# Kernel tuning notes

Measured on AMD Instinct MI355X. Metric: run time of the kernel, lower is better.

The kernel has to match this reference:

```python
import jax, jax.numpy as jnp
import numpy as np

D_MODEL = 1024
NUM_HEADS = 16
HEAD_DIM = D_MODEL // NUM_HEADS


def setup_inputs() -> dict:
    key = jax.random.key(0)
    ks = jax.random.split(key, 12)
    B, Lq, Lkv = 4, 1024, 2048
    s = 1.0 / np.sqrt(D_MODEL)
    inp = {
        "decoder_hidden": jax.random.normal(ks[0], (B, Lq, D_MODEL), jnp.float32),
        "encoder_hidden": jax.random.normal(ks[1], (B, Lkv, D_MODEL), jnp.float32),
        "encoder_mask": jnp.ones((B, 1, 1, Lkv), jnp.int32),
        "Wq": jax.random.normal(ks[2], (D_MODEL, D_MODEL), jnp.float32) * s,
        "bq": jnp.zeros((D_MODEL,), jnp.float32),
        "Wk": jax.random.normal(ks[3], (D_MODEL, D_MODEL), jnp.float32) * s,
        "bk": jnp.zeros((D_MODEL,), jnp.float32),
        "Wv": jax.random.normal(ks[4], (D_MODEL, D_MODEL), jnp.float32) * s,
        "bv": jnp.zeros((D_MODEL,), jnp.float32),
        "Wo": jax.random.normal(ks[5], (D_MODEL, D_MODEL), jnp.float32) * s,
        "bo": jnp.zeros((D_MODEL,), jnp.float32),
    }
    return inp


def _split_heads(x):
    # [B, L, D] -> [B, H, L, Dh]
    B, L, _ = x.shape
    return x.reshape(B, L, NUM_HEADS, HEAD_DIM).transpose(0, 2, 1, 3)


def reference(decoder_hidden, encoder_hidden, encoder_mask,
              Wq, bq, Wk, bk, Wv, bv, Wo, bo):
    B, Lq, _ = decoder_hidden.shape
    q = _split_heads(decoder_hidden @ Wq.T + bq)   # [B,H,Lq,Dh]
    k = _split_heads(encoder_hidden @ Wk.T + bk)   # [B,H,Lkv,Dh]
    v = _split_heads(encoder_hidden @ Wv.T + bv)   # [B,H,Lkv,Dh]
    scale = 1.0 / np.sqrt(HEAD_DIM).astype(np.float32)
    scores = jnp.einsum('bhqd,bhkd->bhqk', q, k) * scale  # [B,H,Lq,Lkv]
    scores = jnp.where(encoder_mask == 0, jnp.float32(-jnp.inf), scores)
    attn = jax.nn.softmax(scores, axis=-1)  # dropout is identity in eval mode
    out = jnp.einsum('bhqk,bhkd->bhqd', attn, v)  # [B,H,Lq,Dh]
    out = out.transpose(0, 2, 1, 3).reshape(B, Lq, D_MODEL)
    return out @ Wo.T + bo
```

## Files before the change

### kernel.cpp

```cpp
#include <hip/hip_runtime.h>
#include <hip/hip_bf16.h>
#include <stdint.h>
#include <math.h>

#define B_   4
#define H_   16
#define LQ_  1024
#define LKV_ 2048
#define DM_  1024
#define DH_  64

typedef __attribute__((ext_vector_type(8))) __bf16 bf16x8;
typedef __attribute__((ext_vector_type(4))) float  f32x4;
typedef __attribute__((ext_vector_type(16))) float f32x16;
typedef __attribute__((ext_vector_type(8))) short  short8;
typedef __attribute__((ext_vector_type(2))) unsigned uint2v;

__device__ __forceinline__ void gload_lds16(const void* g, void* l) {
  __builtin_amdgcn_global_load_lds(
      (const __attribute__((address_space(1))) void*)g,
      (__attribute__((address_space(3))) void*)l, 16, 0, 0);
}

__device__ __forceinline__ void drain_vmem() {
  asm volatile("s_waitcnt vmcnt(0)" ::: "memory");
  __builtin_amdgcn_sched_barrier(0);
}

#if __has_builtin(__builtin_amdgcn_exp2f)
__device__ __forceinline__ float EXP2(float x) { return __builtin_amdgcn_exp2f(x); }
#else
__device__ __forceinline__ float EXP2(float x) {
  float r; asm("v_exp_f32 %0, %1" : "=v"(r) : "v"(x)); return r;
}
#endif

#if __has_builtin(__builtin_amdgcn_permlane32_swap)
__device__ __forceinline__ void xswap(unsigned& a, unsigned& b) {
  uint2v r = __builtin_amdgcn_permlane32_swap(a, b, false, false);
  a = r[0]; b = r[1];
}
#else
__device__ __forceinline__ void xswap(unsigned& a, unsigned& b) {
  unsigned xa = (unsigned)__shfl_xor((int)a, 32);
  unsigned xb = (unsigned)__shfl_xor((int)b, 32);
  bool hi = (threadIdx.x & 32) != 0;
  unsigned na = hi ? xb : a;
  unsigned nb = hi ? b : xa;
  a = na; b = nb;
}
#endif

__device__ __forceinline__ unsigned pack2(float a, float b) {
  unsigned lo = (unsigned)__bfloat16_as_ushort(__float2bfloat16(a));
  unsigned hi = (unsigned)__bfloat16_as_ushort(__float2bfloat16(b));
  return lo | (hi << 16);
}

struct CastArgs {
  const float* src[6];
  __hip_bfloat16* dst[6];
  int n[6];
};

__global__ void cast_multi(CastArgs a) {
  int seg = blockIdx.y;
  int n = a.n[seg];
  int i = (blockIdx.x * blockDim.x + threadIdx.x) * 8;
  if (i >= n) return;
  const float* s = a.src[seg] + i;
  float4 x = *(const float4*)s;
  float4 y = *(const float4*)(s + 4);
  union { short8 v; __hip_bfloat16 h[8]; } u;
  u.h[0] = __float2bfloat16(x.x); u.h[1] = __float2bfloat16(x.y);
  u.h[2] = __float2bfloat16(x.z); u.h[3] = __float2bfloat16(x.w);
  u.h[4] = __float2bfloat16(y.x); u.h[5] = __float2bfloat16(y.y);
  u.h[6] = __float2bfloat16(y.z); u.h[7] = __float2bfloat16(y.w);
  *(short8*)(a.dst[seg] + i) = u.v;
}

__global__ void mask_mul(const int* __restrict__ msk, __hip_bfloat16* __restrict__ mb, int n) {
  int i = blockIdx.x * blockDim.x + threadIdx.x;
  if (i < n) mb[i] = __float2bfloat16(msk[i] ? 1.0f : 0.0f);
}

template<int MODE>
__global__ __launch_bounds__(256, 3)
void gemm_bt(const __hip_bfloat16* __restrict__ A,
             const __hip_bfloat16* __restrict__ Bt,
             const float* __restrict__ bias,
             void* __restrict__ Cout, int M, int N, int K) {
  __shared__ __hip_bfloat16 lA[2][128 * 64];
  __shared__ __hip_bfloat16 lB[2][64 * 64];
  const int tid = threadIdx.x;
  const int lane = tid & 63, wv = tid >> 6;
  const int l16 = lane & 15, lg = lane >> 4;
  const int wm = wv >> 1, wn = wv & 1;
  const int tileM = blockIdx.y * 128, tileN = blockIdx.x * 64;
  const int KB = K * 2;

  f32x4 acc[4][2] = {};
  const int o0 = wv * 1024 + lane * 16;

  auto GSTAGE = [&](int bi, int kt) {
#pragma unroll
    for (int j = 0; j < 4; ++j) {
      int o = o0 + j * 4096;
      int row = o >> 7, col = (o & 127) ^ ((row & 7) << 4);
      gload_lds16((const char*)A + (size_t)(tileM + row) * KB + kt * 2 + col,
                  (char*)lA[bi] + wv * 1024 + j * 4096);
    }
#pragma unroll
    for (int j = 0; j < 2; ++j) {
      int o = o0 + j * 4096;
      int row = o >> 7, col = (o & 127) ^ ((row & 7) << 4);
      gload_lds16((const char*)Bt + (size_t)(tileN + row) * KB + kt * 2 + col,
                  (char*)lB[bi] + wv * 1024 + j * 4096);
    }
  };

  GSTAGE(0, 0);
  drain_vmem();
  __syncthreads();
  int buf = 0;
  const int NT = K / 64;
  for (int t = 0; t < NT; ++t) {
    if (t + 1 < NT) GSTAGE(buf ^ 1, (t + 1) * 64);
    bf16x8 af[4][2], bfr[2][2];
#pragma unroll
    for (int mt = 0; mt < 4; ++mt) {
      const int row = wm * 64 + mt * 16 + l16;
      const int sw = (row & 7) << 4;
#pragma unroll
      for (int kk = 0; kk < 2; ++kk)
        af[mt][kk] = *(const bf16x8*)((const char*)lA[buf] + row * 128 + ((kk * 64 + lg * 16) ^ sw));
    }
#pragma unroll
    for (int nt = 0; nt < 2; ++nt) {
      const int row = wn * 32 + nt * 16 + l16;
      const int sw = (row & 7) << 4;
#pragma unroll
      for (int kk = 0; kk < 2; ++kk)
        bfr[nt][kk] = *(const bf16x8*)((const char*)lB[buf] + row * 128 + ((kk * 64 + lg * 16) ^ sw));
    }
#pragma unroll
    for (int kk = 0; kk < 2; ++kk)
#pragma unroll
      for (int mt = 0; mt < 4; ++mt)
#pragma unroll
        for (int nt = 0; nt < 2; ++nt)
          acc[mt][nt] = __builtin_amdgcn_mfma_f32_16x16x32_bf16(af[mt][kk], bfr[nt][kk], acc[mt][nt], 0, 0, 0);
    drain_vmem();
    __syncthreads();
    buf ^= 1;
  }

#pragma unroll
  for (int mt = 0; mt < 4; ++mt) {
#pragma unroll
    for (int nt = 0; nt < 2; ++nt) {
      int col = tileN + wn * 32 + nt * 16 + l16;
      float bcol = bias[col];
      int row0 = tileM + wm * 64 + mt * 16 + lg * 4;
      f32x4 a = acc[mt][nt];
#pragma unroll
      for (int r = 0; r < 4; ++r) {
        int row = row0 + r;
        float v = a[r] + bcol;
        if (MODE == 0) {
          ((__hip_bfloat16*)Cout)[(size_t)row * N + col] = __float2bfloat16(v);
        } else {
          ((float*)Cout)[(size_t)row * N + col] = v;
        }
      }
    }
  }
}

__global__ __launch_bounds__(256, 3)
void gemm_kv(const __hip_bfloat16* __restrict__ A,
             const __hip_bfloat16* __restrict__ Bt,
             const float* __restrict__ bk,
             const float* __restrict__ bv,
             __hip_bfloat16* __restrict__ Kout,
             __hip_bfloat16* __restrict__ Vtout,
             const int* __restrict__ vmask) {
  const int K = 1024;
  __shared__ __hip_bfloat16 lA[2][128 * 32];
  __shared__ __hip_bfloat16 lB[2][128 * 32];
  const int tid = threadIdx.x;
  const int lane = tid & 63, wv = tid >> 6;
  const int l16 = lane & 15, lg = lane >> 4;
  const int wm = wv >> 1, wn = wv & 1;
  const int tileM = blockIdx.y * 128, tileN = blockIdx.x * 128;
  const int KB = K * 2;

  f32x4 acc[4][4] = {};
  const int o0 = tid * 16;

  auto GSTAGE = [&](int bi, int kt) {
#pragma unroll
    for (int j = 0; j < 2; ++j) {
      int o = o0 + j * 4096;
      int row = o >> 6, col = (o & 63) ^ ((row & 3) << 4);
      gload_lds16((const char*)A + (size_t)(tileM + row) * KB + kt * 2 + col,
                  (char*)lA[bi] + (tid & 192) * 16 + j * 4096);
    }
#pragma unroll
    for (int j = 0; j < 2; ++j) {
      int o = o0 + j * 4096;
      int row = o >> 6, col = (o & 63) ^ ((row & 3) << 4);
      gload_lds16((const char*)Bt + (size_t)(tileN + row) * KB + kt * 2 + col,
                  (char*)lB[bi] + (tid & 192) * 16 + j * 4096);
    }
  };

  GSTAGE(0, 0);
  drain_vmem();
  __syncthreads();
  int buf = 0;
  const int NT = K / 32;
  for (int t = 0; t < NT; ++t) {
    if (t + 1 < NT) GSTAGE(buf ^ 1, (t + 1) * 32);
    bf16x8 af[4], bfr[4];
#pragma unroll
    for (int mt = 0; mt < 4; ++mt) {
      const int row = wm * 64 + mt * 16 + l16;
      af[mt] = *(const bf16x8*)((const char*)lA[buf] + row * 64 + ((lg * 16) ^ ((row & 3) << 4)));
    }
#pragma unroll
    for (int nt = 0; nt < 4; ++nt) {
      const int row = wn * 64 + nt * 16 + l16;
      bfr[nt] = *(const bf16x8*)((const char*)lB[buf] + row * 64 + ((lg * 16) ^ ((row & 3) << 4)));
    }
#pragma unroll
    for (int mt = 0; mt < 4; ++mt)
#pragma unroll
      for (int nt = 0; nt < 4; ++nt)
        acc[mt][nt] = __builtin_amdgcn_mfma_f32_16x16x32_bf16(af[mt], bfr[nt], acc[mt][nt], 0, 0, 0);
    drain_vmem();
    __syncthreads();
    buf ^= 1;
  }

#pragma unroll
  for (int mt = 0; mt < 4; ++mt) {
#pragma unroll
    for (int nt = 0; nt < 4; ++nt) {
      int col = tileN + wn * 64 + nt * 16 + l16;
      int row0 = tileM + wm * 64 + mt * 16 + lg * 4;
      f32x4 a = acc[mt][nt];
      if (col < 1024) {
        float bc = bk[col];
#pragma unroll
        for (int r = 0; r < 4; ++r) {
          int row = row0 + r;
          Kout[(size_t)row * 1024 + col] = __float2bfloat16(a[r] + bc);
        }
      } else {
        int cv = col - 1024;
        float bc = bv[cv];
#pragma unroll
        for (int r = 0; r < 4; ++r) {
          int row = row0 + r;
          int b = row >> 11, kv = row & 2047;
          float v = a[r] + bc;
          if (!vmask[b * 2048 + kv]) v = 0.0f;
          Vtout[((size_t)(b * 1024 + cv)) * 2048 + kv] = __float2bfloat16(v);
        }
      }
    }
  }
}

__global__ __launch_bounds__(256, 2)
void attn_fwd(const __hip_bfloat16* __restrict__ Qg,
              const __hip_bfloat16* __restrict__ Kg,
              const __hip_bfloat16* __restrict__ Vt,
              const __hip_bfloat16* __restrict__ mkb,
              __hip_bfloat16* __restrict__ AO) {
  __shared__ __hip_bfloat16 lK[2][64 * 64];
  __shared__ __hip_bfloat16 lV[2][64 * 64];
  const int tid = threadIdx.x, lane = tid & 63, wv = tid >> 6;
  const int l32 = lane & 31, h = lane >> 5;

  const int blk = blockIdx.x;
  const int c8 = blk & 7, j = blk >> 3;
  const int g8 = c8 * 8 + (j & 7);
  const int qi = j >> 3;
  const int hd = g8 & 15, b = g8 >> 4;
  const int qb = qi * 128;
  const int q0 = qb + wv * 32;

  const char* qbase = (const char*)Qg +
      ((size_t)(b * LQ_ + q0 + l32) * DM_ + hd * DH_ + h * 8) * 2;
  bf16x8 qf[4];
#pragma unroll
  for (int dk = 0; dk < 4; ++dk) qf[dk] = *(const bf16x8*)(qbase + dk * 32);

  f32x16 o[2] = {};
  f32x16 l_acc = {};
  float m2 = -1e30f;
  const float S2 = 0.18033688f;
  const __hip_bfloat16* mrow = mkb + b * LKV_;
  const char* Kbase = (const char*)Kg + ((size_t)(b * LKV_) * DM_ + hd * DH_) * 2;
  const char* Vbase = (const char*)Vt + ((size_t)((b * H_ + hd) * DH_)) * LKV_ * 2;

  const int ofs = wv * 1024 + lane * 16;
  const int r0 = ofs >> 7, c0s = (ofs & 127) ^ ((r0 & 7) << 4);
  const int ofs1 = ofs + 4096;
  const int r1 = ofs1 >> 7, c1s = (ofs1 & 127) ^ ((r1 & 7) << 4);

  auto STAGE = [&](int bi, int kv0) {
    gload_lds16(Kbase + (size_t)(kv0 + r0) * 2048 + c0s, (char*)lK[bi] + wv * 1024);
    gload_lds16(Kbase + (size_t)(kv0 + r1) * 2048 + c1s, (char*)lK[bi] + 4096 + wv * 1024);
    gload_lds16(Vbase + (size_t)r0 * 4096 + kv0 * 2 + c0s, (char*)lV[bi] + wv * 1024);
    gload_lds16(Vbase + (size_t)r1 * 4096 + kv0 * 2 + c1s, (char*)lV[bi] + 4096 + wv * 1024);
  };

  STAGE(0, 0);
  drain_vmem();
  __syncthreads();
  int buf = 0;

  for (int it = 0; it < LKV_ / 64; ++it) {
    const int kv0 = it * 64;
    if (it + 1 < LKV_ / 64) STAGE(buf ^ 1, kv0 + 64);

    f32x16 z[2];
#pragma unroll
    for (int t = 0; t < 2; ++t) {
      z[t] = {};
      const int row = t * 32 + l32;
      const int sw = (row & 7) << 4;
      const char* kp = (const char*)lK[buf] + row * 128;
      __builtin_amdgcn_s_setprio(1);
#pragma unroll
      for (int dk = 0; dk < 4; ++dk) {
        bf16x8 kf = *(const bf16x8*)(kp + ((dk * 32 + h * 16) ^ sw));
        z[t] = __builtin_amdgcn_mfma_f32_32x32x16_bf16(kf, qf[dk], z[t], 0, 0, 0);
      }
      __builtin_amdgcn_s_setprio(0);
    }

    f32x16 zm;
#pragma unroll
    for (int g = 0; g < 16; ++g) zm[g] = fmaxf(z[0][g], z[1][g]);
    float m0 = fmaxf(fmaxf(zm[0], zm[1]), fmaxf(zm[2], zm[3]));
    float m1 = fmaxf(fmaxf(zm[4], zm[5]), fmaxf(zm[6], zm[7]));
    float m4 = fmaxf(fmaxf(zm[8], zm[9]), fmaxf(zm[10], zm[11]));
    float m5 = fmaxf(fmaxf(zm[12], zm[13]), fmaxf(zm[14], zm[15]));
    float mx = fmaxf(fmaxf(m0, m1), fmaxf(m4, m5));
    mx = fmaxf(mx, __shfl_xor(mx, 32));
    float mx2 = mx * S2;

    if (!__all(mx2 - m2 <= 11.5416f)) {
      float mn = fmaxf(m2, mx2);
      float alpha = EXP2(m2 - mn);
      m2 = mn;
#pragma unroll
      for (int g = 0; g < 16; ++g) {
        float a2 = __shfl(alpha, (g & 3) + 8 * (g >> 2) + 4 * h);
        o[0][g] *= a2;
        o[1][g] *= a2;
        l_acc[g] *= a2;
      }
    }

    const float negm2 = -m2;
    unsigned pk[2][4][2];
#pragma unroll
    for (int t = 0; t < 2; ++t)
#pragma unroll
      for (int s = 0; s < 4; ++s) {
        float p0 = EXP2(fmaf(z[t][s * 4 + 0], S2, negm2));
        float p1 = EXP2(fmaf(z[t][s * 4 + 1], S2, negm2));
        float p2 = EXP2(fmaf(z[t][s * 4 + 2], S2, negm2));
        float p3 = EXP2(fmaf(z[t][s * 4 + 3], S2, negm2));
        pk[t][s][0] = pack2(p0, p1);
        pk[t][s][1] = pack2(p2, p3);
      }

#pragma unroll
    for (int c = 0; c < 4; ++c) {
      const int t = c >> 1, cc = c & 1;
      unsigned w0 = pk[t][2 * cc + 0][0], w1 = pk[t][2 * cc + 0][1];
      unsigned w2 = pk[t][2 * cc + 1][0], w3 = pk[t][2 * cc + 1][1];
      xswap(w0, w2);
      xswap(w1, w3);
      union { unsigned w[4]; bf16x8 v; } au;
      au.w[0] = w0; au.w[1] = w1; au.w[2] = w2; au.w[3] = w3;
      bf16x8 mb8 = *(const bf16x8*)(mrow + kv0 + c * 16 + h * 8);
      __builtin_amdgcn_s_setprio(1);
#pragma unroll
      for (int dt = 0; dt < 2; ++dt) {
        const int row = dt * 32 + l32;
        const int sw = (row & 7) << 4;
        bf16x8 vf = *(const bf16x8*)((const char*)lV[buf] + row * 128 + ((c * 32 + h * 16) ^ sw));
        o[dt] = __builtin_amdgcn_mfma_f32_32x32x16_bf16(au.v, vf, o[dt], 0, 0, 0);
      }
      l_acc = __builtin_amdgcn_mfma_f32_32x32x16_bf16(au.v, mb8, l_acc, 0, 0, 0);
      __builtin_amdgcn_s_setprio(0);
    }
    drain_vmem();
    __syncthreads();
    buf ^= 1;
  }

#pragma unroll
  for (int dt = 0; dt < 2; ++dt)
#pragma unroll
    for (int g = 0; g < 16; ++g) {
      int q = (g & 3) + 8 * (g >> 2) + 4 * h;
      AO[(size_t)(b * LQ_ + qb + wv * 32 + q) * DM_ + hd * DH_ + dt * 32 + l32] =
          __float2bfloat16(o[dt][g] / l_acc[g]);
    }
}

extern "C" void kernel_launch(void* const* d_in, const int* in_sizes, int n_in,
                              void* d_out, int out_size, void* d_ws, size_t ws_size,
                              hipStream_t stream) {
  const float* dec = (const float*)d_in[0];
  const float* enc = (const float*)d_in[1];
  const int*   msk = (const int*)d_in[2];
  const float* Wq = (const float*)d_in[3];
  const float* bq = (const float*)d_in[4];
  const float* Wk = (const float*)d_in[5];
  const float* bk = (const float*)d_in[6];
  const float* Wv = (const float*)d_in[7];
  const float* bv = (const float*)d_in[8];
  const float* Wo = (const float*)d_in[9];
  const float* bo = (const float*)d_in[10];

  char* ws = (char*)d_ws;
  __hip_bfloat16* decB = (__hip_bfloat16*)(ws);
  __hip_bfloat16* encB = (__hip_bfloat16*)(ws + 8388608);
  __hip_bfloat16* WqB  = (__hip_bfloat16*)(ws + 25165824);
  __hip_bfloat16* WkvB = (__hip_bfloat16*)(ws + 27262976);
  __hip_bfloat16* WoB  = (__hip_bfloat16*)(ws + 31457280);
  __hip_bfloat16* Qb   = (__hip_bfloat16*)(ws + 33554432);
  __hip_bfloat16* Kb   = (__hip_bfloat16*)(ws + 41943040);
  __hip_bfloat16* Vtb  = (__hip_bfloat16*)(ws + 58720256);
  __hip_bfloat16* AO   = (__hip_bfloat16*)(ws + 75497472);
  __hip_bfloat16* mk2  = (__hip_bfloat16*)(ws + 83886080);

  CastArgs ca;
  ca.src[0] = dec; ca.dst[0] = decB;             ca.n[0] = 4096 * 1024;
  ca.src[1] = enc; ca.dst[1] = encB;             ca.n[1] = 8192 * 1024;
  ca.src[2] = Wq;  ca.dst[2] = WqB;              ca.n[2] = 1024 * 1024;
  ca.src[3] = Wk;  ca.dst[3] = WkvB;             ca.n[3] = 1024 * 1024;
  ca.src[4] = Wv;  ca.dst[4] = WkvB + 1048576;   ca.n[4] = 1024 * 1024;
  ca.src[5] = Wo;  ca.dst[5] = WoB;              ca.n[5] = 1024 * 1024;
  cast_multi<<<dim3(4096, 6), dim3(256), 0, stream>>>(ca);
  mask_mul<<<dim3(32), dim3(256), 0, stream>>>(msk, mk2, B_ * LKV_);

  gemm_bt<0><<<dim3(16, 32), dim3(256), 0, stream>>>(decB, WqB, bq, (void*)Qb, 4096, 1024, 1024);
  gemm_kv<<<dim3(16, 64), dim3(256), 0, stream>>>(encB, WkvB, bk, bv, Kb, Vtb, msk);

  attn_fwd<<<dim3(512), dim3(256), 0, stream>>>(Qb, Kb, Vtb, mk2, AO);

  gemm_bt<2><<<dim3(16, 32), dim3(256), 0, stream>>>(AO, WoB, bo, d_out, 4096, 1024, 1024);
}
```

Measured before the change: 187.4 us.

## Replace LDS-staged attention with single-wave blocks loading K/V into registers

The attention kernel drops its shared-memory double buffer and block barriers. Each 64-thread block now handles 32 queries and reads K and V tiles straight from global memory into registers, prefetching the next K tile while the current one computes. This removes LDS traffic and synchronisation, but each wave now fetches K/V on its own, with no sharing across the four waves that used to share a tile. That raises global/L2 traffic and may expose more load latency.

```diff
diff --git a/kernel.cpp b/kernel.cpp
--- a/kernel.cpp
+++ b/kernel.cpp
@@ -273,15 +273,103 @@
   }
 }
 
-__global__ __launch_bounds__(256, 2)
-void attn_fwd(const __hip_bfloat16* __restrict__ Qg,
+__device__ __forceinline__ void attn_tile(
+    const char* Kb_, const char* Vb_, const __hip_bfloat16* mrow,
+    int kv0, int l32, int h,
+    const bf16x8 (&qf)[4], bf16x8 (&kf_cur)[2][4], bf16x8 (&kf_nxt)[2][4],
+    f32x16 (&o_)[2], f32x16& l_acc, float& m2) {
+  const float S2 = 0.18033688f;
+
+  bf16x8 vf[4][2], mf[4];
+#pragma unroll
+  for (int c = 0; c < 4; ++c) {
+#pragma unroll
+    for (int dt = 0; dt < 2; ++dt)
+      vf[c][dt] = *(const bf16x8*)(Vb_ + (size_t)(dt * 32 + l32) * 4096 + kv0 * 2 + c * 32 + h * 16);
+    mf[c] = *(const bf16x8*)(mrow + kv0 + c * 16 + h * 8);
+  }
+
+  f32x16 z[2];
+#pragma unroll
+  for (int t = 0; t < 2; ++t) {
+    z[t] = {};
+    __builtin_amdgcn_s_setprio(1);
+#pragma unroll
+    for (int dk = 0; dk < 4; ++dk)
+      z[t] = __builtin_amdgcn_mfma_f32_32x32x16_bf16(kf_cur[t][dk], qf[dk], z[t], 0, 0, 0);
+    __builtin_amdgcn_s_setprio(0);
+  }
+
+  const int kvn = (kv0 < (LKV_ - 64)) ? kv0 + 64 : 0;
+#pragma unroll
+  for (int t = 0; t < 2; ++t)
+#pragma unroll
+    for (int dk = 0; dk < 4; ++dk)
+      kf_nxt[t][dk] = *(const bf16x8*)(Kb_ + (size_t)(kvn + t * 32 + l32) * 2048 + dk * 32 + h * 16);
+
+  f32x16 zm;
+#pragma unroll
+  for (int g = 0; g < 16; ++g) zm[g] = fmaxf(z[0][g], z[1][g]);
+  float m0 = fmaxf(fmaxf(zm[0], zm[1]), fmaxf(zm[2], zm[3]));
+  float m1 = fmaxf(fmaxf(zm[4], zm[5]), fmaxf(zm[6], zm[7]));
+  float m4 = fmaxf(fmaxf(zm[8], zm[9]), fmaxf(zm[10], zm[11]));
+  float m5 = fmaxf(fmaxf(zm[12], zm[13]), fmaxf(zm[14], zm[15]));
+  float mx = fmaxf(fmaxf(m0, m1), fmaxf(m4, m5));
+  mx = fmaxf(mx, __shfl_xor(mx, 32));
+  float mx2 = mx * S2;
+
+  if (!__all(mx2 - m2 <= 11.5416f)) {
+    float mn = fmaxf(m2, mx2);
+    float alpha = EXP2(m2 - mn);
+    m2 = mn;
+#pragma unroll
+    for (int g = 0; g < 16; ++g) {
+      float a2 = __shfl(alpha, (g & 3) + 8 * (g >> 2) + 4 * h);
+      o_[0][g] *= a2;
+      o_[1][g] *= a2;
+      l_acc[g] *= a2;
+    }
+  }
+
+  const float negm2 = -m2;
+  unsigned pk[2][4][2];
+#pragma unroll
+  for (int t = 0; t < 2; ++t)
+#pragma unroll
+    for (int s = 0; s < 4; ++s) {
+      float p0 = EXP2(fmaf(z[t][s * 4 + 0], S2, negm2));
+      float p1 = EXP2(fmaf(z[t][s * 4 + 1], S2, negm2));
+      float p2 = EXP2(fmaf(z[t][s * 4 + 2], S2, negm2));
+      float p3 = EXP2(fmaf(z[t][s * 4 + 3], S2, negm2));
+      pk[t][s][0] = pack2(p0, p1);
+      pk[t][s][1] = pack2(p2, p3);
+    }
+
+#pragma unroll
+  for (int c = 0; c < 4; ++c) {
+    const int t = c >> 1, cc = c & 1;
+    unsigned w0 = pk[t][2 * cc + 0][0], w1 = pk[t][2 * cc + 0][1];
+    unsigned w2 = pk[t][2 * cc + 1][0], w3 = pk[t][2 * cc + 1][1];
+    xswap(w0, w2);
+    xswap(w1, w3);
+    union { unsigned w[4]; bf16x8 v; } au;
+    au.w[0] = w0; au.w[1] = w1; au.w[2] = w2; au.w[3] = w3;
+    __builtin_amdgcn_s_setprio(1);
+#pragma unroll
+    for (int dt = 0; dt < 2; ++dt)
+      o_[dt] = __builtin_amdgcn_mfma_f32_32x32x16_bf16(au.v, vf[c][dt], o_[dt], 0, 0, 0);
+    l_acc = __builtin_amdgcn_mfma_f32_32x32x16_bf16(au.v, mf[c], l_acc, 0, 0, 0);
+    __builtin_amdgcn_s_setprio(0);
+  }
+}
+
+__global__ __launch_bounds__(64, 2)
+void attn_reg(const __hip_bfloat16* __restrict__ Qg,
               const __hip_bfloat16* __restrict__ Kg,
               const __hip_bfloat16* __restrict__ Vt,
               const __hip_bfloat16* __restrict__ mkb,
               __hip_bfloat16* __restrict__ AO) {
-  __shared__ __hip_bfloat16 lK[2][64 * 64];
-  __shared__ __hip_bfloat16 lV[2][64 * 64];
-  const int tid = threadIdx.x, lane = tid & 63, wv = tid >> 6;
+  const int lane = threadIdx.x & 63;
   const int l32 = lane & 31, h = lane >> 5;
 
   const int blk = blockIdx.x;
@@ -289,8 +377,7 @@
   const int g8 = c8 * 8 + (j & 7);
   const int qi = j >> 3;
   const int hd = g8 & 15, b = g8 >> 4;
-  const int qb = qi * 128;
-  const int q0 = qb + wv * 32;
+  const int q0 = qi * 32;
 
   const char* qbase = (const char*)Qg +
       ((size_t)(b * LQ_ + q0 + l32) * DM_ + hd * DH_ + h * 8) * 2;
@@ -298,113 +385,24 @@
 #pragma unroll
   for (int dk = 0; dk < 4; ++dk) qf[dk] = *(const bf16x8*)(qbase + dk * 32);
 
-  f32x16 o[2] = {};
+  const char* Kb_ = (const char*)Kg + ((size_t)(b * LKV_) * DM_ + hd * DH_) * 2;
+  const char* Vb_ = (const char*)Vt + ((size_t)((b * H_ + hd) * DH_)) * LKV_ * 2;
+  const __hip_bfloat16* mrow = mkb + b * LKV_;
+
+  bf16x8 kfA[2][4], kfB[2][4];
+#pragma unroll
+  for (int t = 0; t < 2; ++t)
+#pragma unroll
+    for (int dk = 0; dk < 4; ++dk)
+      kfA[t][dk] = *(const bf16x8*)(Kb_ + (size_t)(t * 32 + l32) * 2048 + dk * 32 + h * 16);
+
+  f32x16 o_[2] = {};
   f32x16 l_acc = {};
   float m2 = -1e30f;
-  const float S2 = 0.18033688f;
-  const __hip_bfloat16* mrow = mkb + b * LKV_;
-  const char* Kbase = (const char*)Kg + ((size_t)(b * LKV_) * DM_ + hd * DH_) * 2;
-  const char* Vbase = (const char*)Vt + ((size_t)((b * H_ + hd) * DH_)) * LKV_ * 2;
-
-  const int ofs = wv * 1024 + lane * 16;
-  const int r0 = ofs >> 7, c0s = (ofs & 127) ^ ((r0 & 7) << 4);
-  const int ofs1 = ofs + 4096;
-  const int r1 = ofs1 >> 7, c1s = (ofs1 & 127) ^ ((r1 & 7) << 4);
-
-  auto STAGE = [&](int bi, int kv0) {
-    gload_lds16(Kbase + (size_t)(kv0 + r0) * 2048 + c0s, (char*)lK[bi] + wv * 1024);
-    gload_lds16(Kbase + (size_t)(kv0 + r1) * 2048 + c1s, (char*)lK[bi] + 4096 + wv * 1024);
-    gload_lds16(Vbase + (size_t)r0 * 4096 + kv0 * 2 + c0s, (char*)lV[bi] + wv * 1024);
-    gload_lds16(Vbase + (size_t)r1 * 4096 + kv0 * 2 + c1s, (char*)lV[bi] + 4096 + wv * 1024);
-  };
-
-  STAGE(0, 0);
-  drain_vmem();
-  __syncthreads();
-  int buf = 0;
-
-  for (int it = 0; it < LKV_ / 64; ++it) {
-    const int kv0 = it * 64;
-    if (it + 1 < LKV_ / 64) STAGE(buf ^ 1, kv0 + 64);
-
-    f32x16 z[2];
-#pragma unroll
-    for (int t = 0; t < 2; ++t) {
-      z[t] = {};
-      const int row = t * 32 + l32;
-      const int sw = (row & 7) << 4;
-      const char* kp = (const char*)lK[buf] + row * 128;
-      __builtin_amdgcn_s_setprio(1);
-#pragma unroll
-      for (int dk = 0; dk < 4; ++dk) {
-        bf16x8 kf = *(const bf16x8*)(kp + ((dk * 32 + h * 16) ^ sw));
-        z[t] = __builtin_amdgcn_mfma_f32_32x32x16_bf16(kf, qf[dk], z[t], 0, 0, 0);
-      }
-      __builtin_amdgcn_s_setprio(0);
-    }
-
-    f32x16 zm;
-#pragma unroll
-    for (int g = 0; g < 16; ++g) zm[g] = fmaxf(z[0][g], z[1][g]);
-    float m0 = fmaxf(fmaxf(zm[0], zm[1]), fmaxf(zm[2], zm[3]));
-    float m1 = fmaxf(fmaxf(zm[4], zm[5]), fmaxf(zm[6], zm[7]));
-    float m4 = fmaxf(fmaxf(zm[8], zm[9]), fmaxf(zm[10], zm[11]));
-    float m5 = fmaxf(fmaxf(zm[12], zm[13]), fmaxf(zm[14], zm[15]));
-    float mx = fmaxf(fmaxf(m0, m1), fmaxf(m4, m5));
-    mx = fmaxf(mx, __shfl_xor(mx, 32));
-    float mx2 = mx * S2;
-
-    if (!__all(mx2 - m2 <= 11.5416f)) {
-      float mn = fmaxf(m2, mx2);
-      float alpha = EXP2(m2 - mn);
-      m2 = mn;
-#pragma unroll
-      for (int g = 0; g < 16; ++g) {
-        float a2 = __shfl(alpha, (g & 3) + 8 * (g >> 2) + 4 * h);
-        o[0][g] *= a2;
-        o[1][g] *= a2;
-        l_acc[g] *= a2;
-      }
-    }
-
-    const float negm2 = -m2;
-    unsigned pk[2][4][2];
-#pragma unroll
-    for (int t = 0; t < 2; ++t)
-#pragma unroll
-      for (int s = 0; s < 4; ++s) {
-        float p0 = EXP2(fmaf(z[t][s * 4 + 0], S2, negm2));
-        float p1 = EXP2(fmaf(z[t][s * 4 + 1], S2, negm2));
-        float p2 = EXP2(fmaf(z[t][s * 4 + 2], S2, negm2));
-        float p3 = EXP2(fmaf(z[t][s * 4 + 3], S2, negm2));
-        pk[t][s][0] = pack2(p0, p1);
-        pk[t][s][1] = pack2(p2, p3);
-      }
-
-#pragma unroll
-    for (int c = 0; c < 4; ++c) {
-      const int t = c >> 1, cc = c & 1;
-      unsigned w0 = pk[t][2 * cc + 0][0], w1 = pk[t][2 * cc + 0][1];
-      unsigned w2 = pk[t][2 * cc + 1][0], w3 = pk[t][2 * cc + 1][1];
-      xswap(w0, w2);
-      xswap(w1, w3);
-      union { unsigned w[4]; bf16x8 v; } au;
-      au.w[0] = w0; au.w[1] = w1; au.w[2] = w2; au.w[3] = w3;
-      bf16x8 mb8 = *(const bf16x8*)(mrow + kv0 + c * 16 + h * 8);
-      __builtin_amdgcn_s_setprio(1);
-#pragma unroll
-      for (int dt = 0; dt < 2; ++dt) {
-        const int row = dt * 32 + l32;
-        const int sw = (row & 7) << 4;
-        bf16x8 vf = *(const bf16x8*)((const char*)lV[buf] + row * 128 + ((c * 32 + h * 16) ^ sw));
-        o[dt] = __builtin_amdgcn_mfma_f32_32x32x16_bf16(au.v, vf, o[dt], 0, 0, 0);
-      }
-      l_acc = __builtin_amdgcn_mfma_f32_32x32x16_bf16(au.v, mb8, l_acc, 0, 0, 0);
-      __builtin_amdgcn_s_setprio(0);
-    }
-    drain_vmem();
-    __syncthreads();
-    buf ^= 1;
+
+  for (int it = 0; it < LKV_ / 64; it += 2) {
+    attn_tile(Kb_, Vb_, mrow, it * 64,      l32, h, qf, kfA, kfB, o_, l_acc, m2);
+    attn_tile(Kb_, Vb_, mrow, it * 64 + 64, l32, h, qf, kfB, kfA, o_, l_acc, m2);
   }
 
 #pragma unroll
@@ -412,8 +410,8 @@
 #pragma unroll
     for (int g = 0; g < 16; ++g) {
       int q = (g & 3) + 8 * (g >> 2) + 4 * h;
-      AO[(size_t)(b * LQ_ + qb + wv * 32 + q) * DM_ + hd * DH_ + dt * 32 + l32] =
-          __float2bfloat16(o[dt][g] / l_acc[g]);
+      AO[(size_t)(b * LQ_ + q0 + q) * DM_ + hd * DH_ + dt * 32 + l32] =
+          __float2bfloat16(o_[dt][g] / l_acc[g]);
     }
 }
 
@@ -457,7 +455,7 @@
   gemm_bt<0><<<dim3(16, 32), dim3(256), 0, stream>>>(decB, WqB, bq, (void*)Qb, 4096, 1024, 1024);
   gemm_kv<<<dim3(16, 64), dim3(256), 0, stream>>>(encB, WkvB, bk, bv, Kb, Vtb, msk);
 
-  attn_fwd<<<dim3(512), dim3(256), 0, stream>>>(Qb, Kb, Vtb, mk2, AO);
+  attn_reg<<<dim3(2048), dim3(64), 0, stream>>>(Qb, Kb, Vtb, mk2, AO);
 
   gemm_bt<2><<<dim3(16, 32), dim3(256), 0, stream>>>(AO, WoB, bo, d_out, 4096, 1024, 1024);
 }
```

After: 247.3 us. 1.32x slower.

## Merge Q and KV projections into one launch; widen attention KV tile to 128

Applied to the files above, without the earlier changes.

The Q projection GEMM is folded into the KV GEMM kernel as one 1-D grid of 1280 blocks. The first 256 blocks compute Q tiles and the rest compute K/V tiles, which removes a launch and lets the two GEMMs fill the machine together. The attention kernel now stages 128 KV rows per iteration instead of 64. This halves the loop trips and the barriers, and does the softmax max/rescale once per 128 keys. In exchange it doubles LDS use (64KB across both buffers) and increases register pressure, which may lower occupancy.

```diff
diff --git a/kernel.cpp b/kernel.cpp
--- a/kernel.cpp
+++ b/kernel.cpp
@@ -178,13 +178,17 @@
 }
 
 __global__ __launch_bounds__(256, 3)
-void gemm_kv(const __hip_bfloat16* __restrict__ A,
-             const __hip_bfloat16* __restrict__ Bt,
-             const float* __restrict__ bk,
-             const float* __restrict__ bv,
-             __hip_bfloat16* __restrict__ Kout,
-             __hip_bfloat16* __restrict__ Vtout,
-             const int* __restrict__ vmask) {
+void gemm_qkv(const __hip_bfloat16* __restrict__ decB,
+              const __hip_bfloat16* __restrict__ WqB,
+              const float* __restrict__ bq,
+              const __hip_bfloat16* __restrict__ encB,
+              const __hip_bfloat16* __restrict__ WkvB,
+              const float* __restrict__ bk,
+              const float* __restrict__ bv,
+              __hip_bfloat16* __restrict__ Qout,
+              __hip_bfloat16* __restrict__ Kout,
+              __hip_bfloat16* __restrict__ Vtout,
+              const int* __restrict__ vmask) {
   const int K = 1024;
   __shared__ __hip_bfloat16 lA[2][128 * 32];
   __shared__ __hip_bfloat16 lB[2][128 * 32];
@@ -192,7 +196,20 @@
   const int lane = tid & 63, wv = tid >> 6;
   const int l16 = lane & 15, lg = lane >> 4;
   const int wm = wv >> 1, wn = wv & 1;
-  const int tileM = blockIdx.y * 128, tileN = blockIdx.x * 128;
+
+  const int bid = blockIdx.x;
+  const bool isQ = bid < 256;
+  int tileM, tileN;
+  const __hip_bfloat16 *A, *Bt;
+  if (isQ) {
+    int t = bid;
+    tileN = (t & 7) * 128; tileM = (t >> 3) * 128;
+    A = decB; Bt = WqB;
+  } else {
+    int t = bid - 256;
+    tileN = (t & 15) * 128; tileM = (t >> 4) * 128;
+    A = encB; Bt = WkvB;
+  }
   const int KB = K * 2;
 
   f32x4 acc[4][4] = {};
@@ -250,7 +267,14 @@
       int col = tileN + wn * 64 + nt * 16 + l16;
       int row0 = tileM + wm * 64 + mt * 16 + lg * 4;
       f32x4 a = acc[mt][nt];
-      if (col < 1024) {
+      if (isQ) {
+        float bc = bq[col];
+#pragma unroll
+        for (int r = 0; r < 4; ++r) {
+          int row = row0 + r;
+          Qout[(size_t)row * 1024 + col] = __float2bfloat16(a[r] + bc);
+        }
+      } else if (col < 1024) {
         float bc = bk[col];
 #pragma unroll
         for (int r = 0; r < 4; ++r) {
@@ -279,8 +303,8 @@
               const __hip_bfloat16* __restrict__ Vt,
               const __hip_bfloat16* __restrict__ mkb,
               __hip_bfloat16* __restrict__ AO) {
-  __shared__ __hip_bfloat16 lK[2][64 * 64];
-  __shared__ __hip_bfloat16 lV[2][64 * 64];
+  __shared__ __hip_bfloat16 lK[2][128 * 64];
+  __shared__ __hip_bfloat16 lV[2][2][64 * 64];
   const int tid = threadIdx.x, lane = tid & 63, wv = tid >> 6;
   const int l32 = lane & 31, h = lane >> 5;
 
@@ -298,7 +322,7 @@
 #pragma unroll
   for (int dk = 0; dk < 4; ++dk) qf[dk] = *(const bf16x8*)(qbase + dk * 32);
 
-  f32x16 o[2] = {};
+  f32x16 o_[2] = {};
   f32x16 l_acc = {};
   float m2 = -1e30f;
   const float S2 = 0.18033688f;
@@ -307,15 +331,24 @@
   const char* Vbase = (const char*)Vt + ((size_t)((b * H_ + hd) * DH_)) * LKV_ * 2;
 
   const int ofs = wv * 1024 + lane * 16;
-  const int r0 = ofs >> 7, c0s = (ofs & 127) ^ ((r0 & 7) << 4);
-  const int ofs1 = ofs + 4096;
-  const int r1 = ofs1 >> 7, c1s = (ofs1 & 127) ^ ((r1 & 7) << 4);
 
   auto STAGE = [&](int bi, int kv0) {
-    gload_lds16(Kbase + (size_t)(kv0 + r0) * 2048 + c0s, (char*)lK[bi] + wv * 1024);
-    gload_lds16(Kbase + (size_t)(kv0 + r1) * 2048 + c1s, (char*)lK[bi] + 4096 + wv * 1024);
-    gload_lds16(Vbase + (size_t)r0 * 4096 + kv0 * 2 + c0s, (char*)lV[bi] + wv * 1024);
-    gload_lds16(Vbase + (size_t)r1 * 4096 + kv0 * 2 + c1s, (char*)lV[bi] + 4096 + wv * 1024);
+#pragma unroll
+    for (int r = 0; r < 4; ++r) {
+      int o = ofs + r * 4096;
+      int row = o >> 7, col = (o & 127) ^ ((row & 7) << 4);
+      gload_lds16(Kbase + (size_t)(kv0 + row) * 2048 + col,
+                  (char*)lK[bi] + wv * 1024 + r * 4096);
+    }
+#pragma unroll
+    for (int s = 0; s < 2; ++s)
+#pragma unroll
+      for (int r = 0; r < 2; ++r) {
+        int o = ofs + r * 4096;
+        int row = o >> 7, col = (o & 127) ^ ((row & 7) << 4);
+        gload_lds16(Vbase + (size_t)row * 4096 + (kv0 + s * 64) * 2 + col,
+                    (char*)lV[bi][s] + wv * 1024 + r * 4096);
+      }
   };
 
   STAGE(0, 0);
@@ -323,13 +356,13 @@
   __syncthreads();
   int buf = 0;
 
-  for (int it = 0; it < LKV_ / 64; ++it) {
-    const int kv0 = it * 64;
-    if (it + 1 < LKV_ / 64) STAGE(buf ^ 1, kv0 + 64);
-
-    f32x16 z[2];
-#pragma unroll
-    for (int t = 0; t < 2; ++t) {
+  for (int it = 0; it < LKV_ / 128; ++it) {
+    const int kv0 = it * 128;
+    if (it + 1 < LKV_ / 128) STAGE(buf ^ 1, kv0 + 128);
+
+    f32x16 z[4];
+#pragma unroll
+    for (int t = 0; t < 4; ++t) {
       z[t] = {};
       const int row = t * 32 + l32;
       const int sw = (row & 7) << 4;
@@ -345,7 +378,8 @@
 
     f32x16 zm;
 #pragma unroll
-    for (int g = 0; g < 16; ++g) zm[g] = fmaxf(z[0][g], z[1][g]);
+    for (int g = 0; g < 16; ++g)
+      zm[g] = fmaxf(fmaxf(z[0][g], z[1][g]), fmaxf(z[2][g], z[3][g]));
     float m0 = fmaxf(fmaxf(zm[0], zm[1]), fmaxf(zm[2], zm[3]));
     float m1 = fmaxf(fmaxf(zm[4], zm[5]), fmaxf(zm[6], zm[7]));
     float m4 = fmaxf(fmaxf(zm[8], zm[9]), fmaxf(zm[10], zm[11]));
@@ -361,16 +395,16 @@
 #pragma unroll
       for (int g = 0; g < 16; ++g) {
         float a2 = __shfl(alpha, (g & 3) + 8 * (g >> 2) + 4 * h);
-        o[0][g] *= a2;
-        o[1][g] *= a2;
+        o_[0][g] *= a2;
+        o_[1][g] *= a2;
         l_acc[g] *= a2;
       }
     }
 
     const float negm2 = -m2;
-    unsigned pk[2][4][2];
-#pragma unroll
-    for (int t = 0; t < 2; ++t)
+    unsigned pk[4][4][2];
+#pragma unroll
+    for (int t = 0; t < 4; ++t)
 #pragma unroll
       for (int s = 0; s < 4; ++s) {
         float p0 = EXP2(fmaf(z[t][s * 4 + 0], S2, negm2));
@@ -382,8 +416,9 @@
       }
 
 #pragma unroll
-    for (int c = 0; c < 4; ++c) {
+    for (int c = 0; c < 8; ++c) {
       const int t = c >> 1, cc = c & 1;
+      const int s = c >> 2, cl = c & 3;
       unsigned w0 = pk[t][2 * cc + 0][0], w1 = pk[t][2 * cc + 0][1];
       unsigned w2 = pk[t][2 * cc + 1][0], w3 = pk[t][2 * cc + 1][1];
       xswap(w0, w2);
@@ -396,8 +431,8 @@
       for (int dt = 0; dt < 2; ++dt) {
         const int row = dt * 32 + l32;
         const int sw = (row & 7) << 4;
-        bf16x8 vf = *(const bf16x8*)((const char*)lV[buf] + row * 128 + ((c * 32 + h * 16) ^ sw));
-        o[dt] = __builtin_amdgcn_mfma_f32_32x32x16_bf16(au.v, vf, o[dt], 0, 0, 0);
+        bf16x8 vf = *(const bf16x8*)((const char*)lV[buf][s] + row * 128 + ((cl * 32 + h * 16) ^ sw));
+        o_[dt] = __builtin_amdgcn_mfma_f32_32x32x16_bf16(au.v, vf, o_[dt], 0, 0, 0);
       }
       l_acc = __builtin_amdgcn_mfma_f32_32x32x16_bf16(au.v, mb8, l_acc, 0, 0, 0);
       __builtin_amdgcn_s_setprio(0);
@@ -413,7 +448,7 @@
     for (int g = 0; g < 16; ++g) {
       int q = (g & 3) + 8 * (g >> 2) + 4 * h;
       AO[(size_t)(b * LQ_ + qb + wv * 32 + q) * DM_ + hd * DH_ + dt * 32 + l32] =
-          __float2bfloat16(o[dt][g] / l_acc[g]);
+          __float2bfloat16(o_[dt][g] / l_acc[g]);
     }
 }
 
@@ -454,8 +489,8 @@
   cast_multi<<<dim3(4096, 6), dim3(256), 0, stream>>>(ca);
   mask_mul<<<dim3(32), dim3(256), 0, stream>>>(msk, mk2, B_ * LKV_);
 
-  gemm_bt<0><<<dim3(16, 32), dim3(256), 0, stream>>>(decB, WqB, bq, (void*)Qb, 4096, 1024, 1024);
-  gemm_kv<<<dim3(16, 64), dim3(256), 0, stream>>>(encB, WkvB, bk, bv, Kb, Vtb, msk);
+  gemm_qkv<<<dim3(1280), dim3(256), 0, stream>>>(decB, WqB, bq, encB, WkvB, bk, bv,
+                                                 Qb, Kb, Vtb, msk);
 
   attn_fwd<<<dim3(512), dim3(256), 0, stream>>>(Qb, Kb, Vtb, mk2, AO);
 
```

New measurement: 185.4 us. Within noise of the previous version (-1.1%).
